# Kernel tuning notes

Hardware: AMD Instinct MI355X
Metric: run time of the kernel (lower is better)

## Reference

```python
import jax, jax.numpy as jnp
import numpy as np

B, L, P, H, OUT = 64, 1024, 64, 256, 128


def setup_inputs() -> dict:
    key = jax.random.key(0)
    ks = jax.random.split(key, 15)
    s = lambda k, shape: jax.random.normal(k, shape, jnp.float32) * 0.05
    return {
        "x": jax.random.normal(ks[0], (B, L, P), jnp.float32),
        # encoder GRU (PyTorch layout: W_ih (3H,P), W_hh (3H,H))
        "W_ih_e": s(ks[1], (3 * H, P)),
        "W_hh_e": s(ks[2], (3 * H, H)),
        "b_ih_e": s(ks[3], (3 * H,)),
        "b_hh_e": s(ks[4], (3 * H,)),
        # decoder GRU (input size = hidden_size)
        "W_ih_d": s(ks[5], (3 * H, H)),
        "W_hh_d": s(ks[6], (3 * H, H)),
        "b_ih_d": s(ks[7], (3 * H,)),
        "b_hh_d": s(ks[8], (3 * H,)),
        # decoder output head Linear(H,1) + sigmoid
        "W_dec_out": s(ks[9], (1, H)),
        "b_dec_out": s(ks[10], (1,)),
        # attn Linear(2H, seq_length) -- only output column 0 is used
        "W_attn": s(ks[11], (L, 2 * H)),
        "b_attn": s(ks[12], (L,)),
        # final out Linear(seq_length, output_size)
        "W_out": s(ks[13], (OUT, L)),
        "b_out": s(ks[14], (OUT,)),
    }


def gru_cell(x_t, h, Wih, Whh, bih, bhh):
    """PyTorch GRU cell math. x_t (B,in), h (B,H) -> h' (B,H)."""
    gi = x_t @ Wih.T + bih  # (B,3H)
    gh = h @ Whh.T + bhh    # (B,3H)
    i_r, i_z, i_n = jnp.split(gi, 3, axis=-1)
    h_r, h_z, h_n = jnp.split(gh, 3, axis=-1)
    r = jax.nn.sigmoid(i_r + h_r)
    z = jax.nn.sigmoid(i_z + h_z)
    n = jnp.tanh(i_n + r * h_n)
    return (1.0 - z) * n + z * h


def reference(x, W_ih_e, W_hh_e, b_ih_e, b_hh_e,
              W_ih_d, W_hh_d, b_ih_d, b_hh_d,
              W_dec_out, b_dec_out, W_attn, b_attn, W_out, b_out):
    Bsz, Lseq, _ = x.shape
    Hdim = W_hh_e.shape[1]

    # --- encoder GRU over time ---
    h0 = jnp.zeros((Bsz, Hdim), x.dtype)

    def enc_step(h, x_t):
        h_new = gru_cell(x_t, h, W_ih_e, W_hh_e, b_ih_e, b_hh_e)
        return h_new, h_new

    last_h, h_seq = jax.lax.scan(enc_step, h0, jnp.swapaxes(x, 0, 1))
    h = jnp.swapaxes(h_seq, 0, 1)  # (B, L, H)

    # Only row 0 of attn matters: original keeps e_ij[:, 0].
    wa_s = W_attn[0, :Hdim]   # (H,)
    wa_h = W_attn[0, Hdim:]   # (H,)
    ba = b_attn[0]
    h_proj = h @ wa_h         # (B, L), precomputed across all j

    def dec_step(s, _):
        # Bahdanau scores vectorized over j
        e = (s @ wa_s)[:, None] + h_proj + ba        # (B, L)
        alpha = jax.nn.softmax(e, axis=1)
        c = jnp.einsum('bl,blh->bh', alpha, h)       # context (B, H)
        s_new = gru_cell(c, s, W_ih_d, W_hh_d, b_ih_d, b_hh_d)
        y_i = jax.nn.sigmoid(s_new @ W_dec_out.T + b_dec_out)[:, 0]  # (B,)
        return s_new, y_i

    _, y_seq = jax.lax.scan(dec_step, last_h, None, length=Lseq)
    y = y_seq.T  # (B, L)
    return y @ W_out.T + b_out  # (B, output_size)
```

## Files before the change

### kernel.cpp

```cpp
#include <hip/hip_runtime.h>

#define Bn  64
#define Ln  1024
#define Pn  64
#define Hn  256
#define THn 768
#define ONn 128

typedef __attribute__((ext_vector_type(8))) short short8;
typedef __attribute__((ext_vector_type(4))) float f32x4;
typedef __attribute__((ext_vector_type(4))) int   i32x4;

__device__ __forceinline__ unsigned short f2bf(float f) {
    unsigned u = __float_as_uint(f);
    unsigned r = (u + 0x7FFFu + ((u >> 16) & 1u)) >> 16;
    return (unsigned short)r;
}
__device__ __forceinline__ float bf2f(unsigned short s) {
    return __uint_as_float(((unsigned)s) << 16);
}
__device__ __forceinline__ float sigm(float x) { return 1.0f / (1.0f + __expf(-x)); }
__device__ __forceinline__ float ftanh(float x) { return 1.0f - 2.0f / (__expf(2.0f * x) + 1.0f); }

__device__ __forceinline__ short8 pack8(const float* __restrict__ p) {
    const float4 f0 = *(const float4*)p;
    const float4 f1 = *(const float4*)(p + 4);
    short8 r;
    r[0] = (short)f2bf(f0.x); r[1] = (short)f2bf(f0.y);
    r[2] = (short)f2bf(f0.z); r[3] = (short)f2bf(f0.w);
    r[4] = (short)f2bf(f1.x); r[5] = (short)f2bf(f1.y);
    r[6] = (short)f2bf(f1.z); r[7] = (short)f2bf(f1.w);
    return r;
}

__global__ __launch_bounds__(256) void k1_gi(const float* __restrict__ x,
        const float* __restrict__ Wih, const float* __restrict__ bih,
        const float* __restrict__ bhh, unsigned short* __restrict__ gi) {
    const int tid = threadIdx.x;
    const int wv = tid >> 6;
    const int lane = tid & 63;
    const int l15 = lane & 15;
    const int grp = lane >> 4;
    const long row0 = (long)blockIdx.x * 128;

    short8 wf[12][2];
#pragma unroll
    for (int tn = 0; tn < 12; ++tn) {
        const int col = 192 * wv + 16 * tn + l15;
#pragma unroll
        for (int tk = 0; tk < 2; ++tk)
            wf[tn][tk] = pack8(Wih + (long)col * Pn + 32 * tk + 8 * grp);
    }
    float biasv[12];
#pragma unroll
    for (int tn = 0; tn < 12; ++tn) {
        const int col = 192 * wv + 16 * tn + l15;
        biasv[tn] = bih[col] + (col < 512 ? bhh[col] : 0.0f);
    }

    for (int m = 0; m < 8; ++m) {
        const long arow = row0 + 16 * m + l15;
        short8 af[2];
#pragma unroll
        for (int tk = 0; tk < 2; ++tk)
            af[tk] = pack8(x + arow * Pn + 32 * tk + 8 * grp);
#pragma unroll
        for (int tn = 0; tn < 12; ++tn) {
            f32x4 z4 = {0.f, 0.f, 0.f, 0.f};
            f32x4 acc = __builtin_amdgcn_mfma_f32_16x16x32_bf16(af[0], wf[tn][0], z4, 0, 0, 0);
            acc = __builtin_amdgcn_mfma_f32_16x16x32_bf16(af[1], wf[tn][1], acc, 0, 0, 0);
#pragma unroll
            for (int r = 0; r < 4; ++r) {
                const long row = row0 + 16 * m + 4 * grp + r;
                gi[row * THn + 192 * wv + 16 * tn + l15] = f2bf(acc[r] + biasv[tn]);
            }
        }
    }
}

template<int DEC>
__global__ __launch_bounds__(512, 2) void k_rec(
    const float* __restrict__ Whh, const float* __restrict__ bhh,
    const unsigned short* __restrict__ gi_bf,
    const float* __restrict__ gi_c,
    const float* __restrict__ s0,
    unsigned short* __restrict__ h_seq,
    float* __restrict__ s_seq,
    float* __restrict__ last_h)
{
    const int b = blockIdx.x;
    const int tid = threadIdx.x;
    const int wv = tid >> 6;
    const int lane = tid & 63;
    const int l15 = lane & 15;
    const int grp = lane >> 4;
    const int hb = 32 * wv;
    const int jj = grp & 1;
    const int unit = hb + 16 * jj + l15;

    __shared__ i32x4 hbuf4[2][16];
    char* const hb8 = (char*)hbuf4;

    i32x4 wf[6][4];
    float swq[6];
#pragma unroll
    for (int tn = 0; tn < 6; ++tn) {
        const int g = tn >> 1, j = tn & 1;
        const int col = 256 * g + hb + 16 * j + l15;
        const float* wp = Whh + (long)col * Hn + 16 * grp;
        float amax = 0.0f;
#pragma unroll
        for (int tk = 0; tk < 4; ++tk) {
            const float* p = wp + 64 * tk;
#pragma unroll
            for (int q = 0; q < 4; ++q) {
                const float4 f = ((const float4*)p)[q];
                amax = fmaxf(amax, fmaxf(fmaxf(fabsf(f.x), fabsf(f.y)),
                                         fmaxf(fabsf(f.z), fabsf(f.w))));
            }
        }
        amax = fmaxf(amax, __shfl_xor(amax, 16));
        amax = fmaxf(amax, __shfl_xor(amax, 32));
        amax = fmaxf(amax, 1e-20f);
        const float inv_sw = 127.0f / amax;
        swq[tn] = amax * (1.0f / (127.0f * 127.0f));
#pragma unroll
        for (int tk = 0; tk < 4; ++tk) {
            const float* p = wp + 64 * tk;
            i32x4 r;
#pragma unroll
            for (int q = 0; q < 4; ++q) {
                const float4 f = ((const float4*)p)[q];
                const int b0 = (int)rintf(f.x * inv_sw) & 255;
                const int b1 = (int)rintf(f.y * inv_sw) & 255;
                const int b2 = (int)rintf(f.z * inv_sw) & 255;
                const int b3 = (int)rintf(f.w * inv_sw) & 255;
                r[q] = b0 | (b1 << 8) | (b2 << 16) | (b3 << 24);
            }
            wf[tn][tk] = r;
        }
    }
    const float swr = jj ? swq[1] : swq[0];
    const float swz = jj ? swq[3] : swq[2];
    const float swn = jj ? swq[5] : swq[4];
    const float bhn = bhh[512 + unit];

    float hprev;
    unsigned short giA[3], giB[3];
    float gic[3];

    const unsigned short* gl = nullptr;
    unsigned short* hsp = nullptr;
    float* ssp = nullptr;

    if (!DEC) {
        hprev = 0.0f;
        if (tid < 128) ((int*)hbuf4)[tid] = 0;
        gl = gi_bf + (long)b * Ln * THn + unit;
#pragma unroll
        for (int g = 0; g < 3; ++g) giA[g] = gl[256 * g];
        hsp = h_seq + (long)b * Ln * Hn + unit;
    } else {
        hprev = s0[b * Hn + unit];
        if (tid < 256) hb8[tid] = (char)(int)rintf(s0[b * Hn + tid] * 127.0f);
        const float* gd = gi_c + (long)b * THn;
#pragma unroll
        for (int g = 0; g < 3; ++g) gic[g] = gd[256 * g + unit];
        ssp = s_seq + (long)b * Ln * Hn + unit;
    }
    __syncthreads();

    auto step = [&](int t, unsigned short (&gU)[3], unsigned short (&gP)[3]) {
        const int par = t & 1;
        const int nxt = par ^ 1;
        if (!DEC) {
            gl += THn;
#pragma unroll
            for (int g = 0; g < 3; ++g) gP[g] = gl[256 * g];
        }
        i32x4 acc[6];
#pragma unroll
        for (int tk = 0; tk < 4; ++tk) {
            const i32x4 af = *(const i32x4*)&hb8[par * 256 + 64 * tk + 16 * grp];
            if (tk == 0) {
                const i32x4 zi = {0, 0, 0, 0};
#pragma unroll
                for (int tn = 0; tn < 6; ++tn)
                    acc[tn] = __builtin_amdgcn_mfma_i32_16x16x64_i8(af, wf[tn][0], zi, 0, 0, 0);
            } else {
#pragma unroll
                for (int tn = 0; tn < 6; ++tn)
                    acc[tn] = __builtin_amdgcn_mfma_i32_16x16x64_i8(af, wf[tn][tk], acc[tn], 0, 0, 0);
            }
        }
        const int ar = jj ? acc[1][0] : acc[0][0];
        const int az = jj ? acc[3][0] : acc[2][0];
        const int an = jj ? acc[5][0] : acc[4][0];
        const float gir = DEC ? gic[0] : bf2f(gU[0]);
        const float giz = DEC ? gic[1] : bf2f(gU[1]);
        const float gin = DEC ? gic[2] : bf2f(gU[2]);
        const float r = sigm((float)ar * swr + gir);
        const float z = sigm((float)az * swz + giz);
        const float n = ftanh(gin + r * ((float)an * swn + bhn));
        const float hnew = (1.0f - z) * n + z * hprev;
        hprev = hnew;
        if (grp < 2) {
            hb8[nxt * 256 + unit] = (char)(int)rintf(hnew * 127.0f);
            if (!DEC) hsp[0] = f2bf(hnew);
            else      ssp[0] = hnew;
        }
        if (!DEC) hsp += Hn; else ssp += Hn;
        asm volatile("s_waitcnt lgkmcnt(0)\n\ts_barrier" ::: "memory");
    };

    for (int t = 0; t < Ln; t += 2) {
        step(t, giA, giB);
        step(t + 1, giB, giA);
    }

    if (!DEC) {
        if (grp < 2) last_h[b * Hn + unit] = hprev;
    }
}

__global__ __launch_bounds__(256) void k3_ctx(const unsigned short* __restrict__ h_seq,
        const float* __restrict__ Wattn, const float* __restrict__ Wihd,
        const float* __restrict__ bihd, const float* __restrict__ bhhd,
        float* __restrict__ gi_d) {
    const int b = blockIdx.x;
    const int tid = threadIdx.x;
    const int wv = tid >> 6, lane = tid & 63;
    __shared__ float alpha[Ln];
    __shared__ float red[8];
    __shared__ float cbuf[Hn];
    __shared__ float wah[Hn];

    wah[tid] = Wattn[Hn + tid];
    __syncthreads();

    const unsigned short* hb_ = h_seq + (long)b * Ln * Hn;
    const float4 wv4 = ((const float4*)wah)[lane];

    for (int it = 0; it < 64; ++it) {
        const int lbase = it * 16 + wv * 4;
        const uint2 w0 = ((const uint2*)(hb_ + (long)(lbase + 0) * Hn))[lane];
        const uint2 w1 = ((const uint2*)(hb_ + (long)(lbase + 1) * Hn))[lane];
        const uint2 w2 = ((const uint2*)(hb_ + (long)(lbase + 2) * Hn))[lane];
        const uint2 w3 = ((const uint2*)(hb_ + (long)(lbase + 3) * Hn))[lane];
        float p0 = __uint_as_float(w0.x << 16) * wv4.x + __uint_as_float(w0.x & 0xffff0000u) * wv4.y
                 + __uint_as_float(w0.y << 16) * wv4.z + __uint_as_float(w0.y & 0xffff0000u) * wv4.w;
        float p1 = __uint_as_float(w1.x << 16) * wv4.x + __uint_as_float(w1.x & 0xffff0000u) * wv4.y
                 + __uint_as_float(w1.y << 16) * wv4.z + __uint_as_float(w1.y & 0xffff0000u) * wv4.w;
        float p2 = __uint_as_float(w2.x << 16) * wv4.x + __uint_as_float(w2.x & 0xffff0000u) * wv4.y
                 + __uint_as_float(w2.y << 16) * wv4.z + __uint_as_float(w2.y & 0xffff0000u) * wv4.w;
        float p3 = __uint_as_float(w3.x << 16) * wv4.x + __uint_as_float(w3.x & 0xffff0000u) * wv4.y
                 + __uint_as_float(w3.y << 16) * wv4.z + __uint_as_float(w3.y & 0xffff0000u) * wv4.w;
#pragma unroll
        for (int s = 1; s < 64; s <<= 1) {
            p0 += __shfl_xor(p0, s);
            p1 += __shfl_xor(p1, s);
            p2 += __shfl_xor(p2, s);
            p3 += __shfl_xor(p3, s);
        }
        if (lane == 0) {
            alpha[lbase + 0] = p0; alpha[lbase + 1] = p1;
            alpha[lbase + 2] = p2; alpha[lbase + 3] = p3;
        }
    }
    __syncthreads();

    const float4 hp4 = ((const float4*)alpha)[tid];
    float m = fmaxf(fmaxf(hp4.x, hp4.y), fmaxf(hp4.z, hp4.w));
#pragma unroll
    for (int s = 1; s < 64; s <<= 1) m = fmaxf(m, __shfl_xor(m, s));
    if (lane == 0) red[wv] = m;
    __syncthreads();
    m = fmaxf(fmaxf(red[0], red[1]), fmaxf(red[2], red[3]));
    const float e0 = __expf(hp4.x - m), e1 = __expf(hp4.y - m);
    const float e2 = __expf(hp4.z - m), e3 = __expf(hp4.w - m);
    float ss = e0 + e1 + e2 + e3;
#pragma unroll
    for (int s = 1; s < 64; s <<= 1) ss += __shfl_xor(ss, s);
    if (lane == 0) red[4 + wv] = ss;
    __syncthreads();
    const float inv = 1.0f / (red[4] + red[5] + red[6] + red[7]);
    ((float4*)alpha)[tid] = make_float4(e0 * inv, e1 * inv, e2 * inv, e3 * inv);
    __syncthreads();

    float accv = 0.0f;
    const unsigned short* hs = hb_ + tid;
    for (int l = 0; l < Ln; ++l) accv += alpha[l] * bf2f(hs[(long)l * Hn]);
    cbuf[tid] = accv;
    __syncthreads();

    for (int c = wv; c < THn; c += 4) {
        const float4 wr = ((const float4*)(Wihd + (long)c * Hn))[lane];
        const float4 cc = ((const float4*)cbuf)[lane];
        float p = wr.x * cc.x + wr.y * cc.y + wr.z * cc.z + wr.w * cc.w;
#pragma unroll
        for (int s = 1; s < 64; s <<= 1) p += __shfl_xor(p, s);
        if (lane == 0)
            gi_d[(long)b * THn + c] = p + bihd[c] + (c < 512 ? bhhd[c] : 0.0f);
    }
}

__global__ __launch_bounds__(256) void k5_out(const float* __restrict__ s_seq,
        const float* __restrict__ Wdec, const float* __restrict__ bdec,
        const float* __restrict__ Wout, const float* __restrict__ bout,
        float* __restrict__ out) {
    const int b = blockIdx.x;
    const int tid = threadIdx.x, wv = tid >> 6, lane = tid & 63;
    __shared__ float yl[Ln];
    __shared__ float wd[Hn];
    wd[tid] = Wdec[tid];
    __syncthreads();

    const float* sb = s_seq + (long)b * Ln * Hn;
    const float4 wd4 = ((const float4*)wd)[lane];
    const float bd = bdec[0];

    for (int it = 0; it < 64; ++it) {
        const int lbase = it * 16 + wv * 4;
        const float4 v0 = ((const float4*)(sb + (long)(lbase + 0) * Hn))[lane];
        const float4 v1 = ((const float4*)(sb + (long)(lbase + 1) * Hn))[lane];
        const float4 v2 = ((const float4*)(sb + (long)(lbase + 2) * Hn))[lane];
        const float4 v3 = ((const float4*)(sb + (long)(lbase + 3) * Hn))[lane];
        float p0 = v0.x * wd4.x + v0.y * wd4.y + v0.z * wd4.z + v0.w * wd4.w;
        float p1 = v1.x * wd4.x + v1.y * wd4.y + v1.z * wd4.z + v1.w * wd4.w;
        float p2 = v2.x * wd4.x + v2.y * wd4.y + v2.z * wd4.z + v2.w * wd4.w;
        float p3 = v3.x * wd4.x + v3.y * wd4.y + v3.z * wd4.z + v3.w * wd4.w;
#pragma unroll
        for (int s = 1; s < 64; s <<= 1) {
            p0 += __shfl_xor(p0, s);
            p1 += __shfl_xor(p1, s);
            p2 += __shfl_xor(p2, s);
            p3 += __shfl_xor(p3, s);
        }
        if (lane == 0) {
            yl[lbase + 0] = sigm(p0 + bd); yl[lbase + 1] = sigm(p1 + bd);
            yl[lbase + 2] = sigm(p2 + bd); yl[lbase + 3] = sigm(p3 + bd);
        }
    }
    __syncthreads();

    for (int o = wv; o < ONn; o += 4) {
        const float* wr = Wout + (long)o * Ln;
        float p = 0.0f;
#pragma unroll
        for (int i = 0; i < 16; ++i) p += yl[lane + 64 * i] * wr[lane + 64 * i];
#pragma unroll
        for (int s = 1; s < 64; s <<= 1) p += __shfl_xor(p, s);
        if (lane == 0) out[b * ONn + o] = p + bout[o];
    }
}

extern "C" void kernel_launch(void* const* d_in, const int* in_sizes, int n_in,
                              void* d_out, int out_size, void* d_ws, size_t ws_size,
                              hipStream_t stream) {
    const float* x      = (const float*)d_in[0];
    const float* Wih_e  = (const float*)d_in[1];
    const float* Whh_e  = (const float*)d_in[2];
    const float* bih_e  = (const float*)d_in[3];
    const float* bhh_e  = (const float*)d_in[4];
    const float* Wih_d  = (const float*)d_in[5];
    const float* Whh_d  = (const float*)d_in[6];
    const float* bih_d  = (const float*)d_in[7];
    const float* bhh_d  = (const float*)d_in[8];
    const float* Wdec   = (const float*)d_in[9];
    const float* bdec   = (const float*)d_in[10];
    const float* Wattn  = (const float*)d_in[11];
    const float* Wout   = (const float*)d_in[13];
    const float* bout   = (const float*)d_in[14];
    float* out = (float*)d_out;

    char* ws = (char*)d_ws;
    unsigned short* gi_e  = (unsigned short*)ws;
    unsigned short* h_seq = (unsigned short*)(ws + 100663296);
    float* last_h = (float*)(ws + 134217728);
    float* gi_d   = (float*)(ws + 134283264);
    float* s_seq  = (float*)ws;

    k1_gi<<<512, 256, 0, stream>>>(x, Wih_e, bih_e, bhh_e, gi_e);
    k_rec<0><<<Bn, 512, 0, stream>>>(Whh_e, bhh_e, gi_e, nullptr, nullptr,
                                     h_seq, nullptr, last_h);
    k3_ctx<<<Bn, 256, 0, stream>>>(h_seq, Wattn, Wih_d, bih_d, bhh_d, gi_d);
    k_rec<1><<<Bn, 512, 0, stream>>>(Whh_d, bhh_d, nullptr, gi_d, last_h,
                                     nullptr, s_seq, nullptr);
    k5_out<<<Bn, 256, 0, stream>>>(s_seq, Wdec, bdec, Wout, bout, out);
}
```

Measured before the change: 1.669 ms.

## Pack two batch rows per workgroup and use per-group LDS counter barriers

The recurrent GRU kernel now runs two independent batch rows in one 1024-thread workgroup, with eight waves per row. The full-workgroup s_barrier is replaced by a per-row LDS atomic counter barrier that spins with s_sleep, so each row's waves synchronize only with each other. The aim is to let the two rows' step latencies overlap on one CU and to decouple their synchronization. The cost is that only half as many CUs are used. Two rows also compete for the same SIMDs and registers, and the software spin barrier may have higher latency than the hardware barrier.

```diff
diff --git a/kernel.cpp b/kernel.cpp
--- a/kernel.cpp
+++ b/kernel.cpp
@@ -79,7 +79,7 @@
 }
 
 template<int DEC>
-__global__ __launch_bounds__(512, 2) void k_rec(
+__global__ __launch_bounds__(1024) void k_rec(
     const float* __restrict__ Whh, const float* __restrict__ bhh,
     const unsigned short* __restrict__ gi_bf,
     const float* __restrict__ gi_c,
@@ -88,18 +88,22 @@
     float* __restrict__ s_seq,
     float* __restrict__ last_h)
 {
-    const int b = blockIdx.x;
-    const int tid = threadIdx.x;
-    const int wv = tid >> 6;
+    const int tid  = threadIdx.x;
+    const int w    = tid >> 6;
+    const int g2   = w >> 3;
+    const int wg   = w & 7;
+    const int b    = blockIdx.x * 2 + g2;
     const int lane = tid & 63;
-    const int l15 = lane & 15;
-    const int grp = lane >> 4;
-    const int hb = 32 * wv;
-    const int jj = grp & 1;
+    const int l15  = lane & 15;
+    const int grp  = lane >> 4;
+    const int hb   = 32 * wg;
+    const int jj   = grp & 1;
     const int unit = hb + 16 * jj + l15;
 
-    __shared__ i32x4 hbuf4[2][16];
+    __shared__ i32x4 hbuf4[2][2][16];
+    __shared__ int ctrbuf[32];
     char* const hb8 = (char*)hbuf4;
+    int* const ctr = &ctrbuf[g2 * 16];
 
     i32x4 wf[6][4];
     float swq[6];
@@ -153,22 +157,35 @@
     unsigned short* hsp = nullptr;
     float* ssp = nullptr;
 
+    if (tid < 32) ctrbuf[tid] = 0;
     if (!DEC) {
         hprev = 0.0f;
-        if (tid < 128) ((int*)hbuf4)[tid] = 0;
+        hb8[tid] = 0;
         gl = gi_bf + (long)b * Ln * THn + unit;
 #pragma unroll
         for (int g = 0; g < 3; ++g) giA[g] = gl[256 * g];
         hsp = h_seq + (long)b * Ln * Hn + unit;
     } else {
         hprev = s0[b * Hn + unit];
-        if (tid < 256) hb8[tid] = (char)(int)rintf(s0[b * Hn + tid] * 127.0f);
-        const float* gd = gi_c + (long)b * THn;
-#pragma unroll
-        for (int g = 0; g < 3; ++g) gic[g] = gd[256 * g + unit];
+        if (tid < 512) {
+            const int gg = tid >> 8, uu = tid & 255;
+            hb8[gg * 512 + uu] =
+                (char)(int)rintf(s0[(blockIdx.x * 2 + gg) * Hn + uu] * 127.0f);
+        }
+#pragma unroll
+        for (int g = 0; g < 3; ++g) gic[g] = gi_c[(long)b * THn + 256 * g + unit];
         ssp = s_seq + (long)b * Ln * Hn + unit;
     }
     __syncthreads();
+
+    auto gbar = [&](int tgt) {
+        asm volatile("s_waitcnt lgkmcnt(0)" ::: "memory");
+        if (lane == 0)
+            __hip_atomic_fetch_add(ctr, 1, __ATOMIC_RELEASE, __HIP_MEMORY_SCOPE_WORKGROUP);
+        while (__hip_atomic_load(ctr, __ATOMIC_ACQUIRE, __HIP_MEMORY_SCOPE_WORKGROUP) < tgt)
+            __builtin_amdgcn_s_sleep(1);
+        __builtin_amdgcn_sched_barrier(0);
+    };
 
     auto step = [&](int t, unsigned short (&gU)[3], unsigned short (&gP)[3]) {
         const int par = t & 1;
@@ -181,7 +198,7 @@
         i32x4 acc[6];
 #pragma unroll
         for (int tk = 0; tk < 4; ++tk) {
-            const i32x4 af = *(const i32x4*)&hb8[par * 256 + 64 * tk + 16 * grp];
+            const i32x4 af = *(const i32x4*)&hb8[g2 * 512 + par * 256 + 64 * tk + 16 * grp];
             if (tk == 0) {
                 const i32x4 zi = {0, 0, 0, 0};
 #pragma unroll
@@ -205,12 +222,12 @@
         const float hnew = (1.0f - z) * n + z * hprev;
         hprev = hnew;
         if (grp < 2) {
-            hb8[nxt * 256 + unit] = (char)(int)rintf(hnew * 127.0f);
+            hb8[g2 * 512 + nxt * 256 + unit] = (char)(int)rintf(hnew * 127.0f);
             if (!DEC) hsp[0] = f2bf(hnew);
             else      ssp[0] = hnew;
         }
         if (!DEC) hsp += Hn; else ssp += Hn;
-        asm volatile("s_waitcnt lgkmcnt(0)\n\ts_barrier" ::: "memory");
+        gbar(8 * t + 8);
     };
 
     for (int t = 0; t < Ln; t += 2) {
@@ -381,10 +398,10 @@
     float* s_seq  = (float*)ws;
 
     k1_gi<<<512, 256, 0, stream>>>(x, Wih_e, bih_e, bhh_e, gi_e);
-    k_rec<0><<<Bn, 512, 0, stream>>>(Whh_e, bhh_e, gi_e, nullptr, nullptr,
-                                     h_seq, nullptr, last_h);
+    k_rec<0><<<Bn / 2, 1024, 0, stream>>>(Whh_e, bhh_e, gi_e, nullptr, nullptr,
+                                          h_seq, nullptr, last_h);
     k3_ctx<<<Bn, 256, 0, stream>>>(h_seq, Wattn, Wih_d, bih_d, bhh_d, gi_d);
-    k_rec<1><<<Bn, 512, 0, stream>>>(Whh_d, bhh_d, nullptr, gi_d, last_h,
-                                     nullptr, s_seq, nullptr);
+    k_rec<1><<<Bn / 2, 1024, 0, stream>>>(Whh_d, bhh_d, nullptr, gi_d, last_h,
+                                          nullptr, s_seq, nullptr);
     k5_out<<<Bn, 256, 0, stream>>>(s_seq, Wdec, bdec, Wout, bout, out);
 }
```

Result: slower. 5.918 ms (+254.6%).

## Split attention-score and output-projection kernels into wider grids

Applied to the files above, without the earlier changes.

The attention score projection (h @ wa_h) and the decoder output sigmoid projection are moved into separate kernels with 512 blocks, each handling a 128-step chunk of one batch row. Before, each ran inside a 64-block kernel. The goal is to spread the memory-bound passes over h_seq and s_seq across more CUs. The cost is two extra kernel launches and round trips through global memory for the intermediate h_proj and y buffers.

```diff
diff --git a/kernel.cpp b/kernel.cpp
--- a/kernel.cpp
+++ b/kernel.cpp
@@ -223,26 +223,20 @@
     }
 }
 
-__global__ __launch_bounds__(256) void k3_ctx(const unsigned short* __restrict__ h_seq,
-        const float* __restrict__ Wattn, const float* __restrict__ Wihd,
-        const float* __restrict__ bihd, const float* __restrict__ bhhd,
-        float* __restrict__ gi_d) {
-    const int b = blockIdx.x;
-    const int tid = threadIdx.x;
-    const int wv = tid >> 6, lane = tid & 63;
-    __shared__ float alpha[Ln];
-    __shared__ float red[8];
-    __shared__ float cbuf[Hn];
+__global__ __launch_bounds__(256) void k3a_scores(const unsigned short* __restrict__ h_seq,
+        const float* __restrict__ Wattn, float* __restrict__ h_proj) {
+    const int bid = blockIdx.x;
+    const int b = bid >> 3, chunk = bid & 7;
+    const int tid = threadIdx.x, wv = tid >> 6, lane = tid & 63;
     __shared__ float wah[Hn];
-
     wah[tid] = Wattn[Hn + tid];
     __syncthreads();
 
     const unsigned short* hb_ = h_seq + (long)b * Ln * Hn;
     const float4 wv4 = ((const float4*)wah)[lane];
 
-    for (int it = 0; it < 64; ++it) {
-        const int lbase = it * 16 + wv * 4;
+    for (int it = 0; it < 8; ++it) {
+        const int lbase = chunk * 128 + it * 16 + wv * 4;
         const uint2 w0 = ((const uint2*)(hb_ + (long)(lbase + 0) * Hn))[lane];
         const uint2 w1 = ((const uint2*)(hb_ + (long)(lbase + 1) * Hn))[lane];
         const uint2 w2 = ((const uint2*)(hb_ + (long)(lbase + 2) * Hn))[lane];
@@ -263,13 +257,26 @@
             p3 += __shfl_xor(p3, s);
         }
         if (lane == 0) {
-            alpha[lbase + 0] = p0; alpha[lbase + 1] = p1;
-            alpha[lbase + 2] = p2; alpha[lbase + 3] = p3;
-        }
-    }
-    __syncthreads();
-
-    const float4 hp4 = ((const float4*)alpha)[tid];
+            float* hp = h_proj + (long)b * Ln + lbase;
+            hp[0] = p0; hp[1] = p1; hp[2] = p2; hp[3] = p3;
+        }
+    }
+}
+
+__global__ __launch_bounds__(256) void k3b_ctx(const float* __restrict__ h_proj,
+        const unsigned short* __restrict__ h_seq, const float* __restrict__ Wihd,
+        const float* __restrict__ bihd, const float* __restrict__ bhhd,
+        float* __restrict__ gi_d) {
+    const int b = blockIdx.x;
+    const int tid = threadIdx.x;
+    const int wv = tid >> 6, lane = tid & 63;
+    __shared__ float alpha[Ln];
+    __shared__ float red[8];
+    __shared__ float cbuf[Hn];
+
+    const unsigned short* hb_ = h_seq + (long)b * Ln * Hn;
+
+    const float4 hp4 = ((const float4*)(h_proj + (long)b * Ln))[tid];
     float m = fmaxf(fmaxf(hp4.x, hp4.y), fmaxf(hp4.z, hp4.w));
 #pragma unroll
     for (int s = 1; s < 64; s <<= 1) m = fmaxf(m, __shfl_xor(m, s));
@@ -304,13 +311,12 @@
     }
 }
 
-__global__ __launch_bounds__(256) void k5_out(const float* __restrict__ s_seq,
+__global__ __launch_bounds__(256) void k5a_y(const float* __restrict__ s_seq,
         const float* __restrict__ Wdec, const float* __restrict__ bdec,
-        const float* __restrict__ Wout, const float* __restrict__ bout,
-        float* __restrict__ out) {
-    const int b = blockIdx.x;
+        float* __restrict__ y) {
+    const int bid = blockIdx.x;
+    const int b = bid >> 3, chunk = bid & 7;
     const int tid = threadIdx.x, wv = tid >> 6, lane = tid & 63;
-    __shared__ float yl[Ln];
     __shared__ float wd[Hn];
     wd[tid] = Wdec[tid];
     __syncthreads();
@@ -319,8 +325,8 @@
     const float4 wd4 = ((const float4*)wd)[lane];
     const float bd = bdec[0];
 
-    for (int it = 0; it < 64; ++it) {
-        const int lbase = it * 16 + wv * 4;
+    for (int it = 0; it < 8; ++it) {
+        const int lbase = chunk * 128 + it * 16 + wv * 4;
         const float4 v0 = ((const float4*)(sb + (long)(lbase + 0) * Hn))[lane];
         const float4 v1 = ((const float4*)(sb + (long)(lbase + 1) * Hn))[lane];
         const float4 v2 = ((const float4*)(sb + (long)(lbase + 2) * Hn))[lane];
@@ -337,10 +343,20 @@
             p3 += __shfl_xor(p3, s);
         }
         if (lane == 0) {
-            yl[lbase + 0] = sigm(p0 + bd); yl[lbase + 1] = sigm(p1 + bd);
-            yl[lbase + 2] = sigm(p2 + bd); yl[lbase + 3] = sigm(p3 + bd);
-        }
-    }
+            float* yp = y + (long)b * Ln + lbase;
+            yp[0] = sigm(p0 + bd); yp[1] = sigm(p1 + bd);
+            yp[2] = sigm(p2 + bd); yp[3] = sigm(p3 + bd);
+        }
+    }
+}
+
+__global__ __launch_bounds__(256) void k5b_out(const float* __restrict__ y,
+        const float* __restrict__ Wout, const float* __restrict__ bout,
+        float* __restrict__ out) {
+    const int b = blockIdx.x;
+    const int tid = threadIdx.x, wv = tid >> 6, lane = tid & 63;
+    __shared__ float yl[Ln];
+    ((float4*)yl)[tid] = ((const float4*)(y + (long)b * Ln))[tid];
     __syncthreads();
 
     for (int o = wv; o < ONn; o += 4) {
@@ -378,13 +394,17 @@
     unsigned short* h_seq = (unsigned short*)(ws + 100663296);
     float* last_h = (float*)(ws + 134217728);
     float* gi_d   = (float*)(ws + 134283264);
+    float* h_proj = (float*)(ws + 134479872);
+    float* y      = (float*)(ws + 134742016);
     float* s_seq  = (float*)ws;
 
     k1_gi<<<512, 256, 0, stream>>>(x, Wih_e, bih_e, bhh_e, gi_e);
     k_rec<0><<<Bn, 512, 0, stream>>>(Whh_e, bhh_e, gi_e, nullptr, nullptr,
                                      h_seq, nullptr, last_h);
-    k3_ctx<<<Bn, 256, 0, stream>>>(h_seq, Wattn, Wih_d, bih_d, bhh_d, gi_d);
+    k3a_scores<<<512, 256, 0, stream>>>(h_seq, Wattn, h_proj);
+    k3b_ctx<<<Bn, 256, 0, stream>>>(h_proj, h_seq, Wih_d, bih_d, bhh_d, gi_d);
     k_rec<1><<<Bn, 512, 0, stream>>>(Whh_d, bhh_d, nullptr, gi_d, last_h,
                                      nullptr, s_seq, nullptr);
-    k5_out<<<Bn, 256, 0, stream>>>(s_seq, Wdec, bdec, Wout, bout, out);
-}
+    k5a_y<<<512, 256, 0, stream>>>(s_seq, Wdec, bdec, y);
+    k5b_out<<<Bn, 256, 0, stream>>>(y, Wout, bout, out);
+}
```

After: 1.628 ms. -2.4%, faster.
